# Performance work log

Measured on AMD Instinct MI355X. Metric: run time of the kernel, lower is better.

Reference implementation:

```python
import jax, jax.numpy as jnp
import numpy as np

B, T, D, H = 2, 2048, 1024, 16
DK = D // H


def setup_inputs() -> dict:
    key = jax.random.key(0)
    ks = jax.random.split(key, 11)
    s = 0.02
    inp = {
        "q": jax.random.normal(ks[0], (B, T, D), jnp.float32),
        "k": jax.random.normal(ks[1], (B, T, D), jnp.float32),
        "v": jax.random.normal(ks[2], (B, T, D), jnp.float32),
        # True = masked (causal), broadcast over batch and heads
        "attn_mask": jnp.triu(jnp.ones((T, T), bool), k=1)[None, None],
        "Wq": jax.random.normal(ks[3], (D, D), jnp.float32) * s,
        "bq": jnp.zeros((D,), jnp.float32),
        "Wk": jax.random.normal(ks[4], (D, D), jnp.float32) * s,
        "bk": jnp.zeros((D,), jnp.float32),
        "Wv": jax.random.normal(ks[5], (D, D), jnp.float32) * s,
        "bv": jnp.zeros((D,), jnp.float32),
        "Wo": jax.random.normal(ks[6], (D, D), jnp.float32) * s,
        "bo": jnp.zeros((D,), jnp.float32),
    }
    return inp


def _split_heads(x):
    # [B,T,D] -> [B,H,T,DK]
    return x.reshape(B, T, H, DK).transpose(0, 2, 1, 3)


def reference(q, k, v, attn_mask, Wq, bq, Wk, bk, Wv, bv, Wo, bo):
    query = _split_heads(q @ Wq.T + bq)
    key_ = _split_heads(k @ Wk.T + bk)
    value = _split_heads(v @ Wv.T + bv)
    scale = 1.0 / jnp.sqrt(jnp.asarray(DK, query.dtype))
    scores = jnp.einsum("bhqd,bhkd->bhqk", query, key_) * scale
    scores = jnp.where(attn_mask, -jnp.inf, scores)
    probs = jax.nn.softmax(scores, axis=-1)  # dropout p=0.0 (eval)
    ctx = jnp.einsum("bhqk,bhkd->bhqd", probs, value)
    ctx = ctx.transpose(0, 2, 1, 3).reshape(B, T, D)
    return ctx @ Wo.T + bo
```

## Files before the change

kernel.cpp:

```cpp
#include <hip/hip_runtime.h>
#include <stdint.h>

#define Bsz 2
#define Tseq 2048
#define Dmodel 1024
#define Hn 16
#define DKd 64

typedef __bf16 bf16;
typedef bf16 bf16x8 __attribute__((ext_vector_type(8)));
typedef float f32x4 __attribute__((ext_vector_type(4)));

__device__ inline void gld_lds16(const void* g, void* l) {
  __builtin_amdgcn_global_load_lds(
      (const __attribute__((address_space(1))) uint32_t*)g,
      (__attribute__((address_space(3))) uint32_t*)l, 16, 0, 0);
}

__device__ inline void pack4_store(bf16* dst, float a, float b, float c, float d) {
  union { bf16 h[4]; uint2 u; } pk;
  pk.h[0] = (bf16)a; pk.h[1] = (bf16)b; pk.h[2] = (bf16)c; pk.h[3] = (bf16)d;
  *(uint2*)dst = pk.u;
}

struct CvtArgs {
  const float* src[7];
  bf16* dst[7];
  int n4[7];
};

__global__ void __launch_bounds__(256) cvt_f32_bf16(CvtArgs a) {
  const int z = blockIdx.y;
  const float4* s = (const float4*)a.src[z];
  uint2* d = (uint2*)a.dst[z];
  const int n4 = a.n4[z];
  for (int i = blockIdx.x * 256 + threadIdx.x; i < n4; i += gridDim.x * 256) {
    float4 v = s[i];
    union { bf16 h[4]; uint2 u; } pk;
    pk.h[0] = (bf16)v.x; pk.h[1] = (bf16)v.y;
    pk.h[2] = (bf16)v.z; pk.h[3] = (bf16)v.w;
    d[i] = pk.u;
  }
}

struct GemmArgs {
  const bf16* A[3];
  const bf16* W[3];
  const float* bias[3];
  void* out[3];
  int mode[3];
  float scale[3];
};

__global__ void __launch_bounds__(256) gemm_qkv(GemmArgs g) {
  const int l = blockIdx.x;
  const int z = l >> 8;
  const int r = l & 255;
  const int mt = (r & 7) * 4 + (r >> 6);
  const int nt = (r >> 3) & 7;
  const bf16* __restrict__ A = g.A[z];
  const bf16* __restrict__ W = g.W[z];
  const float* __restrict__ bias = g.bias[z];
  const int mode = g.mode[z];
  const float scl = g.scale[z];

  __shared__ __align__(16) bf16 As[2][128 * 32];
  __shared__ __align__(16) bf16 Bs[2][128 * 32];

  const int tid = threadIdx.x;
  const int w = tid >> 6, lane = tid & 63;
  const int l15 = lane & 15, quad = lane >> 4;
  const int wm = (w >> 1) * 64, wn = (w & 1) * 64;
  const int m0 = mt * 128, n0 = nt * 128;

  const int c0 = tid, c1 = 256 + tid;
  const int row0 = c0 >> 2, ko0 = (c0 & 3) * 8;
  const int row1 = c1 >> 2, ko1 = (c1 & 3) * 8;

  auto STAGE = [&](int buf, int k0) {
    gld_lds16(A + (size_t)(m0 + row0) * Dmodel + k0 + ko0, (void*)(As[buf] + c0 * 8));
    gld_lds16(W + (size_t)(n0 + row0) * Dmodel + k0 + ko0, (void*)(Bs[buf] + c0 * 8));
    gld_lds16(A + (size_t)(m0 + row1) * Dmodel + k0 + ko1, (void*)(As[buf] + c1 * 8));
    gld_lds16(W + (size_t)(n0 + row1) * Dmodel + k0 + ko1, (void*)(Bs[buf] + c1 * 8));
  };

  f32x4 zero = {0.f, 0.f, 0.f, 0.f};
  f32x4 acc[4][4];
#pragma unroll
  for (int mi = 0; mi < 4; ++mi)
#pragma unroll
    for (int ni = 0; ni < 4; ++ni) acc[mi][ni] = zero;

  STAGE(0, 0);
  __syncthreads();

  for (int t = 0; t < 32; ++t) {
    const int cur = t & 1;
    if (t < 31) STAGE(cur ^ 1, (t + 1) * 32);

    bf16x8 af[4], bfr[4];
#pragma unroll
    for (int i = 0; i < 4; ++i) {
      af[i]  = *(const bf16x8*)(As[cur] + (wm + i * 16 + l15) * 32 + quad * 8);
      bfr[i] = *(const bf16x8*)(Bs[cur] + (wn + i * 16 + l15) * 32 + quad * 8);
    }
#pragma unroll
    for (int mi = 0; mi < 4; ++mi)
#pragma unroll
      for (int ni = 0; ni < 4; ++ni)
        acc[mi][ni] = __builtin_amdgcn_mfma_f32_16x16x32_bf16(af[mi], bfr[ni],
                                                              acc[mi][ni], 0, 0, 0);
    __syncthreads();
  }

#pragma unroll
  for (int mi = 0; mi < 4; ++mi) {
#pragma unroll
    for (int r2 = 0; r2 < 4; ++r2) {
      const int m = m0 + wm + mi * 16 + quad * 4 + r2;
      const int bb = m >> 11, tt = m & 2047;
#pragma unroll
      for (int ni = 0; ni < 4; ++ni) {
        const int n = n0 + wn + ni * 16 + l15;
        const float val = (acc[mi][ni][r2] + bias[n]) * scl;
        bf16* o = (bf16*)g.out[z];
        const int hh = n >> 6, dk = n & 63;
        if (mode == 0) {
          o[((size_t)(bb * Hn + hh) * Tseq + tt) * DKd + dk] = (bf16)val;
        } else {
          o[((size_t)(bb * Hn + hh) * DKd + dk) * Tseq + tt] = (bf16)val;
        }
      }
    }
  }
}

__global__ void __launch_bounds__(256) gemm_out64(const bf16* __restrict__ A,
                                                  const bf16* __restrict__ W,
                                                  const float* __restrict__ bias,
                                                  float* __restrict__ out) {
  const int l = blockIdx.x;
  const int mt = (l & 7) * 8 + (l >> 6);
  const int nt = (l >> 3) & 7;

  __shared__ __align__(16) bf16 As[2][64 * 32];
  __shared__ __align__(16) bf16 Bs[2][128 * 32];

  const int tid = threadIdx.x;
  const int w = tid >> 6, lane = tid & 63;
  const int l15 = lane & 15, quad = lane >> 4;
  const int wm = (w >> 1) * 32, wn = (w & 1) * 64;
  const int m0 = mt * 64, n0 = nt * 128;

  const int c0 = tid, c1 = 256 + tid;
  const int rowA = c0 >> 2, koA = (c0 & 3) * 8;
  const int row0 = c0 >> 2, ko0 = (c0 & 3) * 8;
  const int row1 = c1 >> 2, ko1 = (c1 & 3) * 8;

  auto STAGE = [&](int buf, int k0) {
    gld_lds16(A + (size_t)(m0 + rowA) * Dmodel + k0 + koA, (void*)(As[buf] + c0 * 8));
    gld_lds16(W + (size_t)(n0 + row0) * Dmodel + k0 + ko0, (void*)(Bs[buf] + c0 * 8));
    gld_lds16(W + (size_t)(n0 + row1) * Dmodel + k0 + ko1, (void*)(Bs[buf] + c1 * 8));
  };

  f32x4 zero = {0.f, 0.f, 0.f, 0.f};
  f32x4 acc[2][4];
#pragma unroll
  for (int mi = 0; mi < 2; ++mi)
#pragma unroll
    for (int ni = 0; ni < 4; ++ni) acc[mi][ni] = zero;

  STAGE(0, 0);
  __syncthreads();

  for (int t = 0; t < 32; ++t) {
    const int cur = t & 1;
    if (t < 31) STAGE(cur ^ 1, (t + 1) * 32);

    bf16x8 af[2], bfr[4];
#pragma unroll
    for (int i = 0; i < 2; ++i)
      af[i] = *(const bf16x8*)(As[cur] + (wm + i * 16 + l15) * 32 + quad * 8);
#pragma unroll
    for (int i = 0; i < 4; ++i)
      bfr[i] = *(const bf16x8*)(Bs[cur] + (wn + i * 16 + l15) * 32 + quad * 8);
#pragma unroll
    for (int mi = 0; mi < 2; ++mi)
#pragma unroll
      for (int ni = 0; ni < 4; ++ni)
        acc[mi][ni] = __builtin_amdgcn_mfma_f32_16x16x32_bf16(af[mi], bfr[ni],
                                                              acc[mi][ni], 0, 0, 0);
    __syncthreads();
  }

#pragma unroll
  for (int mi = 0; mi < 2; ++mi)
#pragma unroll
    for (int r = 0; r < 4; ++r) {
      const int m = m0 + wm + mi * 16 + quad * 4 + r;
#pragma unroll
      for (int ni = 0; ni < 4; ++ni) {
        const int n = n0 + wn + ni * 16 + l15;
        out[(size_t)m * Dmodel + n] = acc[mi][ni][r] + bias[n];
      }
    }
}

__global__ void __launch_bounds__(256) attn_fused(const bf16* __restrict__ Q,
                                                  const bf16* __restrict__ K,
                                                  const bf16* __restrict__ Vt,
                                                  bf16* __restrict__ ctx) {
  __shared__ __align__(16) bf16 Ks[8 * 128 * 8];
  __shared__ __align__(16) bf16 Vs[16 * 64 * 8];
  __shared__ __align__(16) bf16 plds[4][16][136];

  const int tid = threadIdx.x;
  const int w = tid >> 6, lane = tid & 63;
  const int l15 = lane & 15, quad = lane >> 4;

  const int l = blockIdx.x;
  const int qt = (Tseq / 64 - 1) - (l >> 5);
  const int hb = l & 31;
  const int h = hb & 15, b = hb >> 4;
  const int bh = b * Hn + h;
  const int qb = qt * 64 + w * 16;

  const bf16* Qb = Q + (size_t)bh * Tseq * DKd;
  const bf16* Kb = K + (size_t)bh * Tseq * DKd;
  const bf16* Vb = Vt + (size_t)bh * DKd * Tseq;

  bf16x8 aq0 = *(const bf16x8*)(Qb + (size_t)(qb + l15) * DKd + quad * 8);
  bf16x8 aq1 = *(const bf16x8*)(Qb + (size_t)(qb + l15) * DKd + 32 + quad * 8);

  f32x4 zero = {0.f, 0.f, 0.f, 0.f};
  f32x4 oacc[4];
#pragma unroll
  for (int nd = 0; nd < 4; ++nd) oacc[nd] = zero;
  f32x4 lacc = zero;

  bf16x8 onesf;
#pragma unroll
  for (int i = 0; i < 8; ++i) onesf[i] = (bf16)1.0f;

  const int qmax = qt * 64 + 48;
  for (int j0 = 0; j0 <= qmax; j0 += 128) {
    __syncthreads();
#pragma unroll
    for (int p = 0; p < 4; ++p) {
      const int c = p * 256 + tid;
      gld_lds16(Kb + (size_t)(j0 + (c & 127)) * DKd + (c >> 7) * 8,
                (void*)(Ks + c * 8));
      gld_lds16(Vb + (size_t)(c & 63) * Tseq + j0 + (c >> 6) * 8,
                (void*)(Vs + c * 8));
    }
    __syncthreads();

    if (j0 + 128 <= qb) {
      f32x4 s[8];
#pragma unroll
      for (int ct = 0; ct < 8; ++ct) s[ct] = zero;
#pragma unroll
      for (int ct = 0; ct < 8; ++ct) {
        bf16x8 bk0 = *(const bf16x8*)(Ks + ((quad)*128 + ct * 16 + l15) * 8);
        bf16x8 bk1 = *(const bf16x8*)(Ks + ((4 + quad) * 128 + ct * 16 + l15) * 8);
        s[ct] = __builtin_amdgcn_mfma_f32_16x16x32_bf16(bk0, aq0, s[ct], 0, 0, 0);
        s[ct] = __builtin_amdgcn_mfma_f32_16x16x32_bf16(bk1, aq1, s[ct], 0, 0, 0);
      }
#pragma unroll
      for (int ct = 0; ct < 8; ++ct)
        pack4_store(&plds[w][l15][ct * 16 + quad * 4],
                    exp2f(s[ct][0]), exp2f(s[ct][1]),
                    exp2f(s[ct][2]), exp2f(s[ct][3]));
#pragma unroll
      for (int kc = 0; kc < 4; ++kc) {
        bf16x8 bp = *(const bf16x8*)(&plds[w][l15][kc * 32 + quad * 8]);
        lacc = __builtin_amdgcn_mfma_f32_16x16x32_bf16(onesf, bp, lacc, 0, 0, 0);
#pragma unroll
        for (int nd = 0; nd < 4; ++nd) {
          bf16x8 bv = *(const bf16x8*)(Vs + ((kc * 4 + quad) * 64 + nd * 16 + l15) * 8);
          oacc[nd] = __builtin_amdgcn_mfma_f32_16x16x32_bf16(bv, bp, oacc[nd], 0, 0, 0);
        }
      }
    } else if (j0 <= qb) {
      const int ctl = ((qb - j0) >> 4) + 1;
      const int kclim = (ctl + 1) >> 1;
      for (int ct = 0; ct < ctl; ++ct) {
        bf16x8 bk0 = *(const bf16x8*)(Ks + ((quad)*128 + ct * 16 + l15) * 8);
        bf16x8 bk1 = *(const bf16x8*)(Ks + ((4 + quad) * 128 + ct * 16 + l15) * 8);
        f32x4 s = zero;
        s = __builtin_amdgcn_mfma_f32_16x16x32_bf16(bk0, aq0, s, 0, 0, 0);
        s = __builtin_amdgcn_mfma_f32_16x16x32_bf16(bk1, aq1, s, 0, 0, 0);
        float p[4];
#pragma unroll
        for (int r = 0; r < 4; ++r) {
          p[r] = exp2f(s[r]);
          if (ct == ctl - 1 && (j0 + ct * 16 + quad * 4 + r > qb + l15)) p[r] = 0.f;
        }
        pack4_store(&plds[w][l15][ct * 16 + quad * 4], p[0], p[1], p[2], p[3]);
      }
      if (ctl < 8)
        pack4_store(&plds[w][l15][ctl * 16 + quad * 4], 0.f, 0.f, 0.f, 0.f);
      for (int kc = 0; kc < kclim; ++kc) {
        bf16x8 bp = *(const bf16x8*)(&plds[w][l15][kc * 32 + quad * 8]);
        lacc = __builtin_amdgcn_mfma_f32_16x16x32_bf16(onesf, bp, lacc, 0, 0, 0);
#pragma unroll
        for (int nd = 0; nd < 4; ++nd) {
          bf16x8 bv = *(const bf16x8*)(Vs + ((kc * 4 + quad) * 64 + nd * 16 + l15) * 8);
          oacc[nd] = __builtin_amdgcn_mfma_f32_16x16x32_bf16(bv, bp, oacc[nd], 0, 0, 0);
        }
      }
    }
  }

  const float inv = 1.0f / lacc[0];
  bf16* cb = ctx + (size_t)(b * Tseq + qb + l15) * Dmodel + h * DKd + quad * 4;
#pragma unroll
  for (int nd = 0; nd < 4; ++nd)
    pack4_store(cb + nd * 16, oacc[nd][0] * inv, oacc[nd][1] * inv,
                oacc[nd][2] * inv, oacc[nd][3] * inv);
}

extern "C" void kernel_launch(void* const* d_in, const int* in_sizes, int n_in,
                              void* d_out, int out_size, void* d_ws, size_t ws_size,
                              hipStream_t stream) {
  const float* q = (const float*)d_in[0];
  const float* k = (const float*)d_in[1];
  const float* v = (const float*)d_in[2];
  const float* Wq = (const float*)d_in[4];
  const float* bq = (const float*)d_in[5];
  const float* Wk = (const float*)d_in[6];
  const float* bk = (const float*)d_in[7];
  const float* Wv = (const float*)d_in[8];
  const float* bv = (const float*)d_in[9];
  const float* Wo = (const float*)d_in[10];
  const float* bo = (const float*)d_in[11];

  char* ws = (char*)d_ws;
  const size_t MB = 1024 * 1024;
  bf16* Wq_b = (bf16*)(ws + 0 * MB);
  bf16* Wk_b = (bf16*)(ws + 2 * MB);
  bf16* Wv_b = (bf16*)(ws + 4 * MB);
  bf16* Wo_b = (bf16*)(ws + 6 * MB);
  bf16* q_b  = (bf16*)(ws + 8 * MB);
  bf16* k_b  = (bf16*)(ws + 16 * MB);
  bf16* v_b  = (bf16*)(ws + 24 * MB);
  bf16* Qh   = (bf16*)(ws + 32 * MB);
  bf16* Kh   = (bf16*)(ws + 40 * MB);
  bf16* Vt   = (bf16*)(ws + 48 * MB);
  bf16* ctx  = (bf16*)(ws + 8 * MB);

  const int NACT4 = (Bsz * Tseq * Dmodel) / 4;
  const int NW4 = (Dmodel * Dmodel) / 4;

  CvtArgs ca;
  ca.src[0] = q;  ca.dst[0] = q_b;  ca.n4[0] = NACT4;
  ca.src[1] = k;  ca.dst[1] = k_b;  ca.n4[1] = NACT4;
  ca.src[2] = v;  ca.dst[2] = v_b;  ca.n4[2] = NACT4;
  ca.src[3] = Wq; ca.dst[3] = Wq_b; ca.n4[3] = NW4;
  ca.src[4] = Wk; ca.dst[4] = Wk_b; ca.n4[4] = NW4;
  ca.src[5] = Wv; ca.dst[5] = Wv_b; ca.n4[5] = NW4;
  ca.src[6] = Wo; ca.dst[6] = Wo_b; ca.n4[6] = NW4;
  cvt_f32_bf16<<<dim3(512, 7), 256, 0, stream>>>(ca);

  const float SC = 0.125f * 1.4426950408889634f;
  GemmArgs ga;
  ga.A[0] = q_b; ga.W[0] = Wq_b; ga.bias[0] = bq; ga.out[0] = Qh; ga.mode[0] = 0; ga.scale[0] = SC;
  ga.A[1] = k_b; ga.W[1] = Wk_b; ga.bias[1] = bk; ga.out[1] = Kh; ga.mode[1] = 0; ga.scale[1] = 1.f;
  ga.A[2] = v_b; ga.W[2] = Wv_b; ga.bias[2] = bv; ga.out[2] = Vt; ga.mode[2] = 1; ga.scale[2] = 1.f;
  gemm_qkv<<<dim3(768), 256, 0, stream>>>(ga);

  attn_fused<<<dim3((Tseq / 64) * Hn * Bsz), 256, 0, stream>>>(Qh, Kh, Vt, ctx);

  gemm_out64<<<dim3(512), 256, 0, stream>>>(ctx, Wo_b, bo, (float*)d_out);
}
```

Baseline: 236.9 us.

## Fuse fp32-to-bf16 activation conversion into QKV GEMM loads; unroll attention PV loop

The QKV GEMM now loads fp32 activations straight into LDS with an XOR swizzle and converts them to bf16 when building fragments. This removes the separate conversion pass over q, k and v and its intermediate bf16 buffers, so the conversion kernel only handles the weights. In exchange the A tile in LDS doubles in size and each fragment read needs two float4 loads plus conversion work. Separately, the attention PV loop is fully unrolled to 4 iterations with a guard on the live count.

```diff
diff --git a/kernel.cpp b/kernel.cpp
--- a/kernel.cpp
+++ b/kernel.cpp
@@ -23,10 +23,17 @@
   *(uint2*)dst = pk.u;
 }
 
+__device__ inline bf16x8 cvt8(float4 a, float4 b) {
+  bf16x8 r;
+  r[0] = (bf16)a.x; r[1] = (bf16)a.y; r[2] = (bf16)a.z; r[3] = (bf16)a.w;
+  r[4] = (bf16)b.x; r[5] = (bf16)b.y; r[6] = (bf16)b.z; r[7] = (bf16)b.w;
+  return r;
+}
+
 struct CvtArgs {
-  const float* src[7];
-  bf16* dst[7];
-  int n4[7];
+  const float* src[4];
+  bf16* dst[4];
+  int n4[4];
 };
 
 __global__ void __launch_bounds__(256) cvt_f32_bf16(CvtArgs a) {
@@ -44,7 +51,7 @@
 }
 
 struct GemmArgs {
-  const bf16* A[3];
+  const float* A[3];
   const bf16* W[3];
   const float* bias[3];
   void* out[3];
@@ -58,13 +65,13 @@
   const int r = l & 255;
   const int mt = (r & 7) * 4 + (r >> 6);
   const int nt = (r >> 3) & 7;
-  const bf16* __restrict__ A = g.A[z];
+  const float* __restrict__ A = g.A[z];
   const bf16* __restrict__ W = g.W[z];
   const float* __restrict__ bias = g.bias[z];
   const int mode = g.mode[z];
   const float scl = g.scale[z];
 
-  __shared__ __align__(16) bf16 As[2][128 * 32];
+  __shared__ __align__(16) float Asf[2][128 * 32];
   __shared__ __align__(16) bf16 Bs[2][128 * 32];
 
   const int tid = threadIdx.x;
@@ -77,10 +84,18 @@
   const int row0 = c0 >> 2, ko0 = (c0 & 3) * 8;
   const int row1 = c1 >> 2, ko1 = (c1 & 3) * 8;
 
-  auto STAGE = [&](int buf, int k0) {
-    gld_lds16(A + (size_t)(m0 + row0) * Dmodel + k0 + ko0, (void*)(As[buf] + c0 * 8));
+  auto STAGE_A = [&](int buf, int k0) {
+#pragma unroll
+    for (int p = 0; p < 4; ++p) {
+      const int c = p * 256 + tid;
+      const int row = c >> 3;
+      const int cc = (c & 7) ^ (row & 7);
+      gld_lds16(A + (size_t)(m0 + row) * Dmodel + k0 + cc * 4,
+                (void*)(Asf[buf] + c * 4));
+    }
+  };
+  auto STAGE_W = [&](int buf, int k0) {
     gld_lds16(W + (size_t)(n0 + row0) * Dmodel + k0 + ko0, (void*)(Bs[buf] + c0 * 8));
-    gld_lds16(A + (size_t)(m0 + row1) * Dmodel + k0 + ko1, (void*)(As[buf] + c1 * 8));
     gld_lds16(W + (size_t)(n0 + row1) * Dmodel + k0 + ko1, (void*)(Bs[buf] + c1 * 8));
   };
 
@@ -91,17 +106,25 @@
 #pragma unroll
     for (int ni = 0; ni < 4; ++ni) acc[mi][ni] = zero;
 
-  STAGE(0, 0);
+  STAGE_A(0, 0);
+  STAGE_W(0, 0);
   __syncthreads();
 
   for (int t = 0; t < 32; ++t) {
     const int cur = t & 1;
-    if (t < 31) STAGE(cur ^ 1, (t + 1) * 32);
+    if (t < 31) {
+      STAGE_A(cur ^ 1, (t + 1) * 32);
+      STAGE_W(cur ^ 1, (t + 1) * 32);
+    }
 
     bf16x8 af[4], bfr[4];
 #pragma unroll
     for (int i = 0; i < 4; ++i) {
-      af[i]  = *(const bf16x8*)(As[cur] + (wm + i * 16 + l15) * 32 + quad * 8);
+      const int row = wm + i * 16 + l15;
+      const int x = row & 7;
+      const float4 lo = *(const float4*)(Asf[cur] + row * 32 + (((quad << 1)    ) ^ x) * 4);
+      const float4 hi = *(const float4*)(Asf[cur] + row * 32 + (((quad << 1) | 1) ^ x) * 4);
+      af[i]  = cvt8(lo, hi);
       bfr[i] = *(const bf16x8*)(Bs[cur] + (wn + i * 16 + l15) * 32 + quad * 8);
     }
 #pragma unroll
@@ -300,13 +323,16 @@
       }
       if (ctl < 8)
         pack4_store(&plds[w][l15][ctl * 16 + quad * 4], 0.f, 0.f, 0.f, 0.f);
-      for (int kc = 0; kc < kclim; ++kc) {
-        bf16x8 bp = *(const bf16x8*)(&plds[w][l15][kc * 32 + quad * 8]);
-        lacc = __builtin_amdgcn_mfma_f32_16x16x32_bf16(onesf, bp, lacc, 0, 0, 0);
-#pragma unroll
-        for (int nd = 0; nd < 4; ++nd) {
-          bf16x8 bv = *(const bf16x8*)(Vs + ((kc * 4 + quad) * 64 + nd * 16 + l15) * 8);
-          oacc[nd] = __builtin_amdgcn_mfma_f32_16x16x32_bf16(bv, bp, oacc[nd], 0, 0, 0);
+#pragma unroll
+      for (int kc = 0; kc < 4; ++kc) {
+        if (kc < kclim) {
+          bf16x8 bp = *(const bf16x8*)(&plds[w][l15][kc * 32 + quad * 8]);
+          lacc = __builtin_amdgcn_mfma_f32_16x16x32_bf16(onesf, bp, lacc, 0, 0, 0);
+#pragma unroll
+          for (int nd = 0; nd < 4; ++nd) {
+            bf16x8 bv = *(const bf16x8*)(Vs + ((kc * 4 + quad) * 64 + nd * 16 + l15) * 8);
+            oacc[nd] = __builtin_amdgcn_mfma_f32_16x16x32_bf16(bv, bp, oacc[nd], 0, 0, 0);
+          }
         }
       }
     }
@@ -341,32 +367,25 @@
   bf16* Wk_b = (bf16*)(ws + 2 * MB);
   bf16* Wv_b = (bf16*)(ws + 4 * MB);
   bf16* Wo_b = (bf16*)(ws + 6 * MB);
-  bf16* q_b  = (bf16*)(ws + 8 * MB);
-  bf16* k_b  = (bf16*)(ws + 16 * MB);
-  bf16* v_b  = (bf16*)(ws + 24 * MB);
+  bf16* ctx  = (bf16*)(ws + 8 * MB);
   bf16* Qh   = (bf16*)(ws + 32 * MB);
   bf16* Kh   = (bf16*)(ws + 40 * MB);
   bf16* Vt   = (bf16*)(ws + 48 * MB);
-  bf16* ctx  = (bf16*)(ws + 8 * MB);
-
-  const int NACT4 = (Bsz * Tseq * Dmodel) / 4;
+
   const int NW4 = (Dmodel * Dmodel) / 4;
 
   CvtArgs ca;
-  ca.src[0] = q;  ca.dst[0] = q_b;  ca.n4[0] = NACT4;
-  ca.src[1] = k;  ca.dst[1] = k_b;  ca.n4[1] = NACT4;
-  ca.src[2] = v;  ca.dst[2] = v_b;  ca.n4[2] = NACT4;
-  ca.src[3] = Wq; ca.dst[3] = Wq_b; ca.n4[3] = NW4;
-  ca.src[4] = Wk; ca.dst[4] = Wk_b; ca.n4[4] = NW4;
-  ca.src[5] = Wv; ca.dst[5] = Wv_b; ca.n4[5] = NW4;
-  ca.src[6] = Wo; ca.dst[6] = Wo_b; ca.n4[6] = NW4;
-  cvt_f32_bf16<<<dim3(512, 7), 256, 0, stream>>>(ca);
+  ca.src[0] = Wq; ca.dst[0] = Wq_b; ca.n4[0] = NW4;
+  ca.src[1] = Wk; ca.dst[1] = Wk_b; ca.n4[1] = NW4;
+  ca.src[2] = Wv; ca.dst[2] = Wv_b; ca.n4[2] = NW4;
+  ca.src[3] = Wo; ca.dst[3] = Wo_b; ca.n4[3] = NW4;
+  cvt_f32_bf16<<<dim3(128, 4), 256, 0, stream>>>(ca);
 
   const float SC = 0.125f * 1.4426950408889634f;
   GemmArgs ga;
-  ga.A[0] = q_b; ga.W[0] = Wq_b; ga.bias[0] = bq; ga.out[0] = Qh; ga.mode[0] = 0; ga.scale[0] = SC;
-  ga.A[1] = k_b; ga.W[1] = Wk_b; ga.bias[1] = bk; ga.out[1] = Kh; ga.mode[1] = 0; ga.scale[1] = 1.f;
-  ga.A[2] = v_b; ga.W[2] = Wv_b; ga.bias[2] = bv; ga.out[2] = Vt; ga.mode[2] = 1; ga.scale[2] = 1.f;
+  ga.A[0] = q; ga.W[0] = Wq_b; ga.bias[0] = bq; ga.out[0] = Qh; ga.mode[0] = 0; ga.scale[0] = SC;
+  ga.A[1] = k; ga.W[1] = Wk_b; ga.bias[1] = bk; ga.out[1] = Kh; ga.mode[1] = 0; ga.scale[1] = 1.f;
+  ga.A[2] = v; ga.W[2] = Wv_b; ga.bias[2] = bv; ga.out[2] = Vt; ga.mode[2] = 1; ga.scale[2] = 1.f;
   gemm_qkv<<<dim3(768), 256, 0, stream>>>(ga);
 
   attn_fused<<<dim3((Tseq / 64) * Hn * Bsz), 256, 0, stream>>>(Qh, Kh, Vt, ctx);
```

New measurement: 257.5 us. +8.7%, slower.
